# Performance work log

Measured on AMD Instinct MI355X. Metric: run time of the kernel, lower is better.

Reference implementation:

```python
import jax, jax.numpy as jnp
import numpy as np

EPS = 1e-9
LN_EPS = 1e-5
NORM_EPS = 1e-12


def _roi_proj(pooled, proj_w, proj_b, ln_g, ln_b):
    # pooled: (..., C) -> linear -> layernorm over last dim
    v = jnp.einsum('...c,pc->...p', pooled, proj_w) + proj_b
    mu = v.mean(axis=-1, keepdims=True)
    var = jnp.mean((v - mu) ** 2, axis=-1, keepdims=True)
    return ln_g * (v - mu) / jnp.sqrt(var + LN_EPS) + ln_b


def _l2norm(v):
    n = jnp.sqrt(jnp.sum(v * v, axis=-1, keepdims=True))
    return v / jnp.maximum(n, NORM_EPS)


def setup_inputs() -> dict:
    key = jax.random.key(0)
    ks = jax.random.split(key, 12)
    B, M, N, C, G = 4, 512, 512, 256, 7
    P, H = 32, 32
    x = jax.random.normal(ks[0], (B, M, C, G, G), dtype=jnp.float32)
    prev_x = jax.random.normal(ks[1], (B, N, C, G, G), dtype=jnp.float32)
    match = jax.random.uniform(ks[2], (B, M, N + 1), dtype=jnp.float32)
    proj_w = jax.random.normal(ks[3], (P, C), dtype=jnp.float32) / np.sqrt(C)
    proj_b = jax.random.normal(ks[4], (P,), dtype=jnp.float32) * 0.01
    ln_g = jnp.ones((P,), dtype=jnp.float32)
    ln_b = jnp.zeros((P,), dtype=jnp.float32)
    w1 = jax.random.normal(ks[5], (H, 5), dtype=jnp.float32) / np.sqrt(5)
    b1 = jax.random.normal(ks[6], (H,), dtype=jnp.float32) * 0.01
    w2 = jax.random.normal(ks[7], (1, H), dtype=jnp.float32) / np.sqrt(H)
    b2 = jax.random.normal(ks[8], (1,), dtype=jnp.float32) * 0.01
    return {"x": x, "prev_x": prev_x, "match": match,
            "proj_w": proj_w, "proj_b": proj_b, "ln_g": ln_g, "ln_b": ln_b,
            "w1": w1, "b1": b1, "w2": w2, "b2": b2}


def reference(x, prev_x, match, proj_w, proj_b, ln_g, ln_b, w1, b1, w2, b2):
    # ---- stats from match (torch.no_grad equivalent) ----
    p_dummy = match[..., -1]                      # (B, M)
    real = match[..., :-1]                        # (B, M, N)
    real_mass = real.sum(axis=-1)                 # (B, M)
    top2, _ = jax.lax.top_k(real, 2)              # N >= 2
    p_max = top2[..., 0]
    p_gap = top2[..., 0] - top2[..., 1]
    r = jnp.maximum(real, EPS)
    ent = -jnp.sum(r * jnp.log(r), axis=-1)
    top1 = jnp.argmax(real, axis=-1)              # (B, M)
    has_real = real_mass > EPS
    top1 = jnp.where(has_real, top1, 0)

    # ---- ROI projection (pool -> linear -> layernorm) ----
    # spatial mean pool (AdaptiveAvgPool2d(1)); pooling commutes with gather,
    # so pool prev_x once then gather pooled vectors (same math, less traffic)
    x_pool = x.mean(axis=(-2, -1))                # (B, M, C)
    prev_pool = prev_x.mean(axis=(-2, -1))        # (B, N, C)
    prev_picked = jnp.take_along_axis(prev_pool, top1[..., None], axis=1)  # (B, M, C)

    curr_vec = _roi_proj(x_pool, proj_w, proj_b, ln_g, ln_b)
    prev_vec = _roi_proj(prev_picked, proj_w, proj_b, ln_g, ln_b)
    cos_sim = jnp.sum(_l2norm(curr_vec) * _l2norm(prev_vec), axis=-1)
    cos_sim = jnp.where(has_real, cos_sim, 0.0)

    # ---- tiny MLP gate ----
    feat = jnp.stack([1.0 - p_dummy, p_max, p_gap, -ent, cos_sim], axis=-1)
    feat = jax.lax.stop_gradient(feat.astype(jnp.float32))  # (B, M, 5)
    h = jax.nn.relu(jnp.einsum('bmf,hf->bmh', feat, w1) + b1)
    logit = jnp.einsum('bmh,oh->bmo', h, w2) + b2            # (B, M, 1)
    c = jax.nn.sigmoid(logit)
    no_real = (real_mass <= 1e-6)[..., None]
    c = jnp.where(no_real, 0.0, c)
    c = jnp.clip(c, 0.001, 1.0 - 0.001)
    return c[0]
```

## Files before the change

### kernel.cpp

```cpp
#include <hip/hip_runtime.h>
#include <math.h>

#define C_CH 256
#define GG 49
#define ROW_ELEMS (C_CH * GG)
#define ROW_VEC4  (ROW_ELEMS / 4)
#define NP 32
#define NREAL 512

__global__ __launch_bounds__(256) void gate_fused_kernel(
    const float* __restrict__ x,
    const float* __restrict__ prev_x,
    const float* __restrict__ match,
    const float* __restrict__ proj_w,
    const float* __restrict__ proj_b,
    const float* __restrict__ ln_g,
    const float* __restrict__ ln_b,
    const float* __restrict__ w1,
    const float* __restrict__ b1,
    const float* __restrict__ w2,
    const float* __restrict__ b2,
    float* __restrict__ out)
{
    const int m   = blockIdx.x;
    const int tid = threadIdx.x;

    __shared__ __align__(16) float tile[ROW_ELEMS];
    __shared__ double pooled[C_CH];
    __shared__ double parts[8][NP];
    __shared__ double vecs[2][NP];
    __shared__ int    s_top1;
    __shared__ double s_wmass[4], s_went[4];
    __shared__ float  s_wm1[4], s_wm2[4];
    __shared__ int    s_wi1[4];

    const float* __restrict__ row = match + (size_t)m * (NREAL + 1);
    float v0 = row[tid];
    float v1 = row[tid + 256];

    double mass = (double)v0 + (double)v1;
    double r0 = fmax((double)v0, 1e-9);
    double r1 = fmax((double)v1, 1e-9);
    double entn = r0 * log(r0) + r1 * log(r1);

    float m1, m2; int i1;
    if (v0 >= v1) { m1 = v0; m2 = v1; i1 = tid; }
    else          { m1 = v1; m2 = v0; i1 = tid + 256; }

    #pragma unroll
    for (int mask = 1; mask < 64; mask <<= 1) {
        double o_mass = __shfl_xor(mass, mask, 64);
        double o_ent  = __shfl_xor(entn, mask, 64);
        float  o_m1   = __shfl_xor(m1,   mask, 64);
        float  o_m2   = __shfl_xor(m2,   mask, 64);
        int    o_i1   = __shfl_xor(i1,   mask, 64);
        mass += o_mass; entn += o_ent;
        if (o_m1 > m1)      { m2 = fmaxf(m1, o_m2); m1 = o_m1; i1 = o_i1; }
        else if (o_m1 < m1) { m2 = fmaxf(m2, o_m1); }
        else                { m2 = m1; i1 = (o_i1 < i1) ? o_i1 : i1; }
    }

    const int wid = tid >> 6, lane = tid & 63;
    if (lane == 0) {
        s_wmass[wid] = mass; s_went[wid] = entn;
        s_wm1[wid] = m1; s_wm2[wid] = m2; s_wi1[wid] = i1;
    }
    __syncthreads();
    if (tid == 0) {
        double tmass = s_wmass[0], tent = s_went[0];
        float tm1 = s_wm1[0], tm2 = s_wm2[0]; int ti1 = s_wi1[0];
        for (int w = 1; w < 4; ++w) {
            tmass += s_wmass[w]; tent += s_went[w];
            float om1 = s_wm1[w], om2 = s_wm2[w]; int oi1 = s_wi1[w];
            if (om1 > tm1)      { tm2 = fmaxf(tm1, om2); tm1 = om1; ti1 = oi1; }
            else if (om1 < tm1) { tm2 = fmaxf(tm2, om1); }
            else                { tm2 = tm1; ti1 = (oi1 < ti1) ? oi1 : ti1; }
        }
        s_wmass[0] = tmass; s_went[0] = tent; s_wm1[0] = tm1; s_wm2[0] = tm2;
        s_top1 = (tmass > 1e-9) ? ti1 : 0;
    }
    __syncthreads();
    const int top1 = s_top1;

    for (int phase = 0; phase < 2; ++phase) {
        const float* __restrict__ src =
            (phase == 0) ? (x + (size_t)m * ROW_ELEMS)
                         : (prev_x + (size_t)top1 * ROW_ELEMS);
        const float4* __restrict__ s4 = reinterpret_cast<const float4*>(src);
        float4* t4 = reinterpret_cast<float4*>(tile);
        for (int i = tid; i < ROW_VEC4; i += 256) t4[i] = s4[i];
        __syncthreads();

        {
            const float* p = &tile[tid * GG];
            double s = 0.0;
            #pragma unroll
            for (int j = 0; j < GG; ++j) s += (double)p[j];
            pooled[tid] = s * (1.0 / 49.0);
        }
        __syncthreads();

        {
            const int p = tid & 31, g = tid >> 5;
            const float* __restrict__ wrow = proj_w + p * C_CH + g * 32;
            const double* pl = pooled + g * 32;
            double acc = 0.0;
            #pragma unroll
            for (int c = 0; c < 32; ++c) acc += pl[c] * (double)wrow[c];
            parts[g][p] = acc;
        }
        __syncthreads();

        if (tid < NP) {
            double v = (double)proj_b[tid];
            #pragma unroll
            for (int g = 0; g < 8; ++g) v += parts[g][tid];
            double s = v;
            #pragma unroll
            for (int mask = 1; mask <= 16; mask <<= 1) s += __shfl_xor(s, mask, 64);
            double mu = s * (1.0 / 32.0);
            double d  = v - mu;
            double q  = d * d;
            #pragma unroll
            for (int mask = 1; mask <= 16; mask <<= 1) q += __shfl_xor(q, mask, 64);
            double var = q * (1.0 / 32.0);
            double y = (double)ln_g[tid] * (d / sqrt(var + 1e-5)) + (double)ln_b[tid];
            double yy = y * y;
            #pragma unroll
            for (int mask = 1; mask <= 16; mask <<= 1) yy += __shfl_xor(yy, mask, 64);
            double n = fmax(sqrt(yy), 1e-12);
            vecs[phase][tid] = y / n;
        }
        __syncthreads();
    }

    if (tid == 0) {
        double tmass = s_wmass[0];
        double feat3 = s_went[0];
        float  pm  = s_wm1[0], pm2 = s_wm2[0];
        bool has_real = tmass > 1e-9;

        double cs = 0.0;
        if (has_real) {
            double s = 0.0;
            #pragma unroll
            for (int p = 0; p < NP; ++p) s += vecs[0][p] * vecs[1][p];
            cs = s;
        }
        double p_dummy = (double)row[NREAL];
        double feat[5] = {1.0 - p_dummy, (double)pm, (double)pm - (double)pm2, feat3, cs};

        double logit = (double)b2[0];
        for (int h = 0; h < 32; ++h) {
            double a = (double)b1[h];
            #pragma unroll
            for (int f = 0; f < 5; ++f) a += feat[f] * (double)w1[h * 5 + f];
            if (a > 0.0) logit += a * (double)w2[h];
        }
        double c = 1.0 / (1.0 + exp(-logit));
        if (!(tmass > 1e-6)) c = 0.0;
        c = fmin(fmax(c, 0.001), 0.999);
        out[m] = (float)c;
    }
}

extern "C" void kernel_launch(void* const* d_in, const int* in_sizes, int n_in,
                              void* d_out, int out_size, void* d_ws, size_t ws_size,
                              hipStream_t stream) {
    (void)in_sizes; (void)n_in; (void)d_ws; (void)ws_size; (void)out_size;
    const float* x      = (const float*)d_in[0];
    const float* prev_x = (const float*)d_in[1];
    const float* match  = (const float*)d_in[2];
    const float* proj_w = (const float*)d_in[3];
    const float* proj_b = (const float*)d_in[4];
    const float* ln_g   = (const float*)d_in[5];
    const float* ln_b   = (const float*)d_in[6];
    const float* w1     = (const float*)d_in[7];
    const float* b1     = (const float*)d_in[8];
    const float* w2     = (const float*)d_in[9];
    const float* b2     = (const float*)d_in[10];
    float* out = (float*)d_out;

    gate_fused_kernel<<<dim3(512), dim3(256), 0, stream>>>(
        x, prev_x, match, proj_w, proj_b, ln_g, ln_b, w1, b1, w2, b2, out);
}
```

Measured before the change: 211.2 us.

## Split pooling into separate kernel over all rows, then gate from workspace

Spatial pooling moves out of the fused kernel into its own kernel with 1024 blocks. Each block pools one x row or one prev_x row straight from global memory into a double workspace, with no shared-memory tile staging. The gate kernel then gathers the two pooled vectors and runs both projections and layernorms at the same time using all 256 threads. This frees the large shared-memory tile and serialised phases, which should raise occupancy and memory parallelism. In exchange it pools every prev_x row instead of only the picked ones, adds a second launch, and uses uncoalesced per-thread strided reads.

Result: slower. 215.7 us (+2.1%).

```diff
diff --git a/kernel.cpp b/kernel.cpp
--- a/kernel.cpp
+++ b/kernel.cpp
@@ -4,13 +4,28 @@
 #define C_CH 256
 #define GG 49
 #define ROW_ELEMS (C_CH * GG)
-#define ROW_VEC4  (ROW_ELEMS / 4)
 #define NP 32
 #define NREAL 512
+#define NROWS 512
 
-__global__ __launch_bounds__(256) void gate_fused_kernel(
+__global__ __launch_bounds__(256) void pool_kernel(
     const float* __restrict__ x,
     const float* __restrict__ prev_x,
+    double* __restrict__ pooled)
+{
+    const int b = blockIdx.x;
+    const int c = threadIdx.x;
+    const float* __restrict__ src =
+        ((b < NROWS) ? (x + (size_t)b * ROW_ELEMS)
+                     : (prev_x + (size_t)(b - NROWS) * ROW_ELEMS)) + c * GG;
+    double s = 0.0;
+    #pragma unroll
+    for (int j = 0; j < GG; ++j) s += (double)src[j];
+    pooled[(size_t)b * C_CH + c] = s * (1.0 / 49.0);
+}
+
+__global__ __launch_bounds__(256) void gate_kernel(
+    const double* __restrict__ pooled,
     const float* __restrict__ match,
     const float* __restrict__ proj_w,
     const float* __restrict__ proj_b,
@@ -25,9 +40,8 @@
     const int m   = blockIdx.x;
     const int tid = threadIdx.x;
 
-    __shared__ __align__(16) float tile[ROW_ELEMS];
-    __shared__ double pooled[C_CH];
-    __shared__ double parts[8][NP];
+    __shared__ double spool[2][C_CH];
+    __shared__ double parts[2][4][NP];
     __shared__ double vecs[2][NP];
     __shared__ int    s_top1;
     __shared__ double s_wmass[4], s_went[4];
@@ -82,57 +96,45 @@
     __syncthreads();
     const int top1 = s_top1;
 
-    for (int phase = 0; phase < 2; ++phase) {
-        const float* __restrict__ src =
-            (phase == 0) ? (x + (size_t)m * ROW_ELEMS)
-                         : (prev_x + (size_t)top1 * ROW_ELEMS);
-        const float4* __restrict__ s4 = reinterpret_cast<const float4*>(src);
-        float4* t4 = reinterpret_cast<float4*>(tile);
-        for (int i = tid; i < ROW_VEC4; i += 256) t4[i] = s4[i];
-        __syncthreads();
+    spool[0][tid] = pooled[(size_t)m * C_CH + tid];
+    spool[1][tid] = pooled[(size_t)(NROWS + top1) * C_CH + tid];
+    __syncthreads();
 
-        {
-            const float* p = &tile[tid * GG];
-            double s = 0.0;
-            #pragma unroll
-            for (int j = 0; j < GG; ++j) s += (double)p[j];
-            pooled[tid] = s * (1.0 / 49.0);
-        }
-        __syncthreads();
+    {
+        const int p   = tid & 31;
+        const int g   = (tid >> 5) & 3;
+        const int vec = tid >> 7;
+        const float* __restrict__ wrow = proj_w + p * C_CH + g * 64;
+        const double* pl = &spool[vec][g * 64];
+        double acc = 0.0;
+        #pragma unroll
+        for (int k = 0; k < 64; ++k) acc += pl[k] * (double)wrow[k];
+        parts[vec][g][p] = acc;
+    }
+    __syncthreads();
 
-        {
-            const int p = tid & 31, g = tid >> 5;
-            const float* __restrict__ wrow = proj_w + p * C_CH + g * 32;
-            const double* pl = pooled + g * 32;
-            double acc = 0.0;
-            #pragma unroll
-            for (int c = 0; c < 32; ++c) acc += pl[c] * (double)wrow[c];
-            parts[g][p] = acc;
-        }
-        __syncthreads();
-
-        if (tid < NP) {
-            double v = (double)proj_b[tid];
-            #pragma unroll
-            for (int g = 0; g < 8; ++g) v += parts[g][tid];
-            double s = v;
-            #pragma unroll
-            for (int mask = 1; mask <= 16; mask <<= 1) s += __shfl_xor(s, mask, 64);
-            double mu = s * (1.0 / 32.0);
-            double d  = v - mu;
-            double q  = d * d;
-            #pragma unroll
-            for (int mask = 1; mask <= 16; mask <<= 1) q += __shfl_xor(q, mask, 64);
-            double var = q * (1.0 / 32.0);
-            double y = (double)ln_g[tid] * (d / sqrt(var + 1e-5)) + (double)ln_b[tid];
-            double yy = y * y;
-            #pragma unroll
-            for (int mask = 1; mask <= 16; mask <<= 1) yy += __shfl_xor(yy, mask, 64);
-            double n = fmax(sqrt(yy), 1e-12);
-            vecs[phase][tid] = y / n;
-        }
-        __syncthreads();
+    if (tid < 64) {
+        const int p = tid & 31, vec = tid >> 5;
+        double v = (double)proj_b[p];
+        #pragma unroll
+        for (int g = 0; g < 4; ++g) v += parts[vec][g][p];
+        double s = v;
+        #pragma unroll
+        for (int mask = 1; mask <= 16; mask <<= 1) s += __shfl_xor(s, mask, 32);
+        double mu = s * (1.0 / 32.0);
+        double d  = v - mu;
+        double q  = d * d;
+        #pragma unroll
+        for (int mask = 1; mask <= 16; mask <<= 1) q += __shfl_xor(q, mask, 32);
+        double var = q * (1.0 / 32.0);
+        double y = (double)ln_g[p] * (d / sqrt(var + 1e-5)) + (double)ln_b[p];
+        double yy = y * y;
+        #pragma unroll
+        for (int mask = 1; mask <= 16; mask <<= 1) yy += __shfl_xor(yy, mask, 32);
+        double n = fmax(sqrt(yy), 1e-12);
+        vecs[vec][p] = y / n;
     }
+    __syncthreads();
 
     if (tid == 0) {
         double tmass = s_wmass[0];
@@ -167,7 +169,7 @@
 extern "C" void kernel_launch(void* const* d_in, const int* in_sizes, int n_in,
                               void* d_out, int out_size, void* d_ws, size_t ws_size,
                               hipStream_t stream) {
-    (void)in_sizes; (void)n_in; (void)d_ws; (void)ws_size; (void)out_size;
+    (void)in_sizes; (void)n_in; (void)ws_size; (void)out_size;
     const float* x      = (const float*)d_in[0];
     const float* prev_x = (const float*)d_in[1];
     const float* match  = (const float*)d_in[2];
@@ -180,7 +182,9 @@
     const float* w2     = (const float*)d_in[9];
     const float* b2     = (const float*)d_in[10];
     float* out = (float*)d_out;
+    double* pooled = (double*)d_ws;
 
-    gate_fused_kernel<<<dim3(512), dim3(256), 0, stream>>>(
-        x, prev_x, match, proj_w, proj_b, ln_g, ln_b, w1, b1, w2, b2, out);
+    pool_kernel<<<dim3(2 * NROWS), dim3(256), 0, stream>>>(x, prev_x, pooled);
+    gate_kernel<<<dim3(NROWS), dim3(256), 0, stream>>>(
+        pooled, match, proj_w, proj_b, ln_g, ln_b, w1, b1, w2, b2, out);
 }
```
